# Optimization experiments

Measured on AMD Instinct MI355X. Metric: run time of the kernel, lower is better.

## Reference

```python
import jax, jax.numpy as jnp
import numpy as np

D_MODEL = 1024
NUM_HEADS = 16
D_HEAD = D_MODEL // NUM_HEADS
LN_EPS = 1e-5
ROPE_BASE = 10000.0


def layer_norm(x, w, b=None, eps=LN_EPS):
    mu = jnp.mean(x, axis=-1, keepdims=True)
    var = jnp.mean(jnp.square(x - mu), axis=-1, keepdims=True)
    y = (x - mu) * jax.lax.rsqrt(var + eps) * w
    return y + b if b is not None else y


def _rotate_half(x):
    x1, x2 = jnp.split(x, 2, axis=-1)
    return jnp.concatenate([-x2, x1], axis=-1)


def apply_rotary(q, k):
    # q, k: [B, S, H, Dh]
    s, dh = q.shape[1], q.shape[-1]
    inv_freq = 1.0 / (ROPE_BASE ** (jnp.arange(0, dh, 2, dtype=jnp.float32) / dh))
    t = jnp.arange(s, dtype=jnp.float32)
    freqs = jnp.outer(t, inv_freq)                      # [S, Dh/2]
    emb = jnp.concatenate([freqs, freqs], axis=-1)      # [S, Dh]
    cos = jnp.cos(emb)[None, :, None, :].astype(q.dtype)
    sin = jnp.sin(emb)[None, :, None, :].astype(q.dtype)
    q_rot = q * cos + _rotate_half(q) * sin
    k_rot = k * cos + _rotate_half(k) * sin
    return q_rot, k_rot


def setup_inputs() -> dict:
    key = jax.random.key(0)
    ks = jax.random.split(key, 8)
    B, L, D = 4, 2048, D_MODEL
    x = jax.random.normal(ks[0], (B, L, D), dtype=jnp.float32)
    sequence_id = jnp.sort(jax.random.randint(ks[1], (B, L), 0, 8), axis=-1).astype(jnp.int64)
    scale = 1.0 / np.sqrt(D)
    return {
        "x": x,
        "sequence_id": sequence_id,
        "ln_w": jnp.ones((D,), jnp.float32),
        "ln_b": jnp.zeros((D,), jnp.float32),
        "w_qkv": jax.random.normal(ks[2], (D, 3 * D), jnp.float32) * scale,
        "q_ln_w": jnp.ones((D,), jnp.float32),
        "k_ln_w": jnp.ones((D,), jnp.float32),
        "w_out": jax.random.normal(ks[3], (D, D), jnp.float32) * scale,
    }


def reference(x, sequence_id, ln_w, ln_b, w_qkv, q_ln_w, k_ln_w, w_out):
    B, L, D = x.shape
    H, Dh = NUM_HEADS, D_HEAD
    # fused LayerNorm + QKV projection
    qkv = layer_norm(x, ln_w, ln_b) @ w_qkv              # [B, L, 3D]
    q, k, v = jnp.split(qkv, 3, axis=-1)
    # qk layernorm (scale only, bias=False)
    q = layer_norm(q, q_ln_w)
    k = layer_norm(k, k_ln_w)
    # split heads and apply rotary
    q = q.reshape(B, L, H, Dh)
    k = k.reshape(B, L, H, Dh)
    q, k = apply_rotary(q, k)
    v = v.reshape(B, L, H, Dh)
    # packed-sequence mask: tokens attend only within same sequence id
    mask = (sequence_id[:, :, None] == sequence_id[:, None, :])[:, None, :, :]  # [B,1,L,L]
    scale = 1.0 / np.sqrt(Dh)
    scores = jnp.einsum("bqhd,bkhd->bhqk", q, k) * scale
    scores = jnp.where(mask, scores, jnp.finfo(scores.dtype).min)
    attn = jax.nn.softmax(scores, axis=-1)
    ctx = jnp.einsum("bhqk,bkhd->bqhd", attn, v).reshape(B, L, D)
    return ctx @ w_out
```

## Files before the change

### kernel.cpp

```cpp
#include <hip/hip_runtime.h>
#include <hip/hip_bf16.h>
#include <cstdint>
#include <cstddef>
#include <type_traits>

#define D_MODEL 1024
#define NH      16
#define DH      64
#define LSEQ    2048
#define BATCH   4
#define NTOK    8192
#define K3      3072

typedef __attribute__((ext_vector_type(8))) short  short8;
typedef __attribute__((ext_vector_type(4))) float  floatx4;

__device__ __forceinline__ unsigned short f2bf_bits(float f) {
  __hip_bfloat16 h = __float2bfloat16(f);
  return __builtin_bit_cast(unsigned short, h);
}
__device__ __forceinline__ float bf2f(unsigned short u) {
  return __bfloat162float(__builtin_bit_cast(__hip_bfloat16, u));
}
__device__ __forceinline__ unsigned int pack_bf16(float lo, float hi) {
  return (unsigned int)f2bf_bits(lo) | ((unsigned int)f2bf_bits(hi) << 16);
}

__device__ __forceinline__ void gld_lds16(const void* g, void* l) {
  __builtin_amdgcn_global_load_lds(
      (const __attribute__((address_space(1))) void*)g,
      (__attribute__((address_space(3))) void*)l,
      16, 0, 0);
}

__global__ __launch_bounds__(256)
void transpose_cast(const float* __restrict__ src, __hip_bfloat16* __restrict__ dst,
                    int R, int C) {
  __shared__ float tile[32][33];
  const int c0 = blockIdx.x * 32, r0 = blockIdx.y * 32;
  const int x = threadIdx.x, y = threadIdx.y;
  #pragma unroll
  for (int j = 0; j < 32; j += 8)
    tile[y + j][x] = src[(size_t)(r0 + y + j) * C + c0 + x];
  __syncthreads();
  #pragma unroll
  for (int j = 0; j < 32; j += 8)
    dst[(size_t)(c0 + y + j) * R + r0 + x] = __float2bfloat16(tile[x][y + j]);
}

__global__ __launch_bounds__(256)
void ln_kernel(const float* __restrict__ x, const float* __restrict__ w,
               const float* __restrict__ bb, __hip_bfloat16* __restrict__ h) {
  const int t = blockIdx.x, tid = threadIdx.x;
  const float4 v = reinterpret_cast<const float4*>(x + (size_t)t * D_MODEL)[tid];
  float s  = v.x + v.y + v.z + v.w;
  float ss = v.x*v.x + v.y*v.y + v.z*v.z + v.w*v.w;
  #pragma unroll
  for (int off = 32; off > 0; off >>= 1) {
    s  += __shfl_down(s, off);
    ss += __shfl_down(ss, off);
  }
  __shared__ float red[8];
  if ((tid & 63) == 0) { red[(tid >> 6) * 2] = s; red[(tid >> 6) * 2 + 1] = ss; }
  __syncthreads();
  s  = red[0] + red[2] + red[4] + red[6];
  ss = red[1] + red[3] + red[5] + red[7];
  const float mu  = s * (1.f / D_MODEL);
  const float var = ss * (1.f / D_MODEL) - mu * mu;
  const float rs  = rsqrtf(var + 1e-5f);
  const float4 wv = reinterpret_cast<const float4*>(w)[tid];
  const float4 bv = reinterpret_cast<const float4*>(bb)[tid];
  ushort4 o;
  o.x = f2bf_bits((v.x - mu) * rs * wv.x + bv.x);
  o.y = f2bf_bits((v.y - mu) * rs * wv.y + bv.y);
  o.z = f2bf_bits((v.z - mu) * rs * wv.z + bv.z);
  o.w = f2bf_bits((v.w - mu) * rs * wv.w + bv.w);
  reinterpret_cast<ushort4*>(h + (size_t)t * D_MODEL)[tid] = o;
}

template <typename OutT>
__global__ __launch_bounds__(256, 2)
void gemm_bt(const __hip_bfloat16* __restrict__ A, const __hip_bfloat16* __restrict__ Bt,
             OutT* __restrict__ C, int M, int N, int K) {
  const int tid  = threadIdx.x;
  const int lane = tid & 63;
  const int wave = tid >> 6;
  const int bm = blockIdx.y * 128;
  const int bn = blockIdx.x * 128;
  const int wm = (wave & 1) * 64;
  const int wn = (wave >> 1) * 64;
  const int quad = lane >> 4;
  const int l16  = lane & 15;

  __shared__ __align__(16) __hip_bfloat16 As[128 * 32];
  __shared__ __align__(16) __hip_bfloat16 Bs[128 * 32];

  floatx4 acc[4][4];
  #pragma unroll
  for (int i = 0; i < 4; i++)
    #pragma unroll
    for (int j = 0; j < 4; j++) {
      floatx4 z = {0.f, 0.f, 0.f, 0.f};
      acc[i][j] = z;
    }

  const __hip_bfloat16* Ab = A  + (size_t)bm * K;
  const __hip_bfloat16* Bb = Bt + (size_t)bn * K;
  const int rowa = tid >> 2;
  const int kc   = (tid & 3) * 8;

  for (int k0 = 0; k0 < K; k0 += 32) {
    __syncthreads();
    gld_lds16(Ab + (size_t)rowa        * K + (k0 + kc), (char*)As + tid * 16);
    gld_lds16(Ab + (size_t)(rowa + 64) * K + (k0 + kc), (char*)As + 4096 + tid * 16);
    gld_lds16(Bb + (size_t)rowa        * K + (k0 + kc), (char*)Bs + tid * 16);
    gld_lds16(Bb + (size_t)(rowa + 64) * K + (k0 + kc), (char*)Bs + 4096 + tid * 16);
    __syncthreads();
    short8 af[4], bfr[4];
    #pragma unroll
    for (int i = 0; i < 4; i++)
      af[i] = *reinterpret_cast<const short8*>(As + (wm + i * 16 + l16) * 32 + quad * 8);
    #pragma unroll
    for (int j = 0; j < 4; j++)
      bfr[j] = *reinterpret_cast<const short8*>(Bs + (wn + j * 16 + l16) * 32 + quad * 8);
    #pragma unroll
    for (int i = 0; i < 4; i++)
      #pragma unroll
      for (int j = 0; j < 4; j++)
        acc[i][j] = __builtin_amdgcn_mfma_f32_16x16x32_bf16(af[i], bfr[j], acc[i][j], 0, 0, 0);
  }

  #pragma unroll
  for (int i = 0; i < 4; i++)
    #pragma unroll
    for (int j = 0; j < 4; j++) {
      const int row0 = bm + wm + i * 16 + quad * 4;
      const int col  = bn + wn + j * 16 + l16;
      #pragma unroll
      for (int r = 0; r < 4; r++) {
        if constexpr (std::is_same<OutT, __hip_bfloat16>::value)
          C[(size_t)(row0 + r) * N + col] = __float2bfloat16(acc[i][j][r]);
        else
          C[(size_t)(row0 + r) * N + col] = acc[i][j][r];
      }
    }
}

__global__ __launch_bounds__(256)
void seg_kernel(const int* __restrict__ sid, int* __restrict__ segstart,
                int* __restrict__ segend) {
  const int i = blockIdx.x * 256 + threadIdx.x;
  const int b = i >> 11, l = i & 2047;
  const int* row = sid + (size_t)b * LSEQ;
  const int v = row[l];
  int lo = 0, hi = l;
  while (lo < hi) { int mid = (lo + hi) >> 1; if (row[mid] < v) lo = mid + 1; else hi = mid; }
  segstart[i] = lo;
  lo = l + 1; hi = LSEQ;
  while (lo < hi) { int mid = (lo + hi) >> 1; if (row[mid] <= v) lo = mid + 1; else hi = mid; }
  segend[i] = lo;
}

__global__ __launch_bounds__(256)
void rope_kernel(const unsigned short* __restrict__ qkv, const float* __restrict__ qw,
                 const float* __restrict__ kw, unsigned short* __restrict__ qT,
                 unsigned short* __restrict__ kT, unsigned short* __restrict__ vN) {
  const int t = blockIdx.x, tid = threadIdx.x;
  const int b = t >> 11, l = t & 2047;
  const unsigned short* row = qkv + (size_t)t * K3;
  const ushort4 qu = reinterpret_cast<const ushort4*>(row)[tid];
  const ushort4 ku = reinterpret_cast<const ushort4*>(row + 1024)[tid];
  const ushort4 vu = reinterpret_cast<const ushort4*>(row + 2048)[tid];
  const float4 q4 = make_float4(bf2f(qu.x), bf2f(qu.y), bf2f(qu.z), bf2f(qu.w));
  const float4 k4 = make_float4(bf2f(ku.x), bf2f(ku.y), bf2f(ku.z), bf2f(ku.w));
  float qs  = q4.x + q4.y + q4.z + q4.w;
  float qss = q4.x*q4.x + q4.y*q4.y + q4.z*q4.z + q4.w*q4.w;
  float ks  = k4.x + k4.y + k4.z + k4.w;
  float kss = k4.x*k4.x + k4.y*k4.y + k4.z*k4.z + k4.w*k4.w;
  #pragma unroll
  for (int off = 32; off > 0; off >>= 1) {
    qs  += __shfl_down(qs, off);  qss += __shfl_down(qss, off);
    ks  += __shfl_down(ks, off);  kss += __shfl_down(kss, off);
  }
  __shared__ float red[16];
  const int w = tid >> 6;
  if ((tid & 63) == 0) {
    red[w*4] = qs; red[w*4+1] = qss; red[w*4+2] = ks; red[w*4+3] = kss;
  }
  __syncthreads();
  qs  = red[0] + red[4] + red[8]  + red[12];
  qss = red[1] + red[5] + red[9]  + red[13];
  ks  = red[2] + red[6] + red[10] + red[14];
  kss = red[3] + red[7] + red[11] + red[15];
  const float qmu = qs * (1.f/1024), qvar = qss * (1.f/1024) - qmu*qmu;
  const float qrs = rsqrtf(qvar + 1e-5f);
  const float kmu = ks * (1.f/1024), kvar = kss * (1.f/1024) - kmu*kmu;
  const float krs = rsqrtf(kvar + 1e-5f);

  __shared__ float qn[1024];
  __shared__ float kn[1024];
  const float4 qwv = reinterpret_cast<const float4*>(qw)[tid];
  const float4 kwv = reinterpret_cast<const float4*>(kw)[tid];
  const int d = tid * 4;
  qn[d+0] = (q4.x - qmu) * qrs * qwv.x;
  qn[d+1] = (q4.y - qmu) * qrs * qwv.y;
  qn[d+2] = (q4.z - qmu) * qrs * qwv.z;
  qn[d+3] = (q4.w - qmu) * qrs * qwv.w;
  kn[d+0] = (k4.x - kmu) * krs * kwv.x;
  kn[d+1] = (k4.y - kmu) * krs * kwv.y;
  kn[d+2] = (k4.z - kmu) * krs * kwv.z;
  kn[d+3] = (k4.w - kmu) * krs * kwv.w;
  __syncthreads();

  const int hh = d >> 6, dh = d & 63;
  float oq[4], ok[4];
  #pragma unroll
  for (int i = 0; i < 4; i++) {
    const int dd = dh + i;
    const int j = dd & 31;
    const float th = (float)l * __expf(-(float)j * 0.28782313662425575f);
    const float cs = cosf(th), sn = sinf(th);
    const float qp = (dd < 32) ? -qn[d + i + 32] : qn[d + i - 32];
    const float kp = (dd < 32) ? -kn[d + i + 32] : kn[d + i - 32];
    oq[i] = (qn[d + i] * cs + qp * sn) * 0.125f;
    ok[i] = kn[d + i] * cs + kp * sn;
  }
  const size_t ob = ((size_t)(b * NH + hh) * LSEQ + l) * DH + dh;
  ushort4 pq, pk, pv;
  pq.x = f2bf_bits(oq[0]); pq.y = f2bf_bits(oq[1]); pq.z = f2bf_bits(oq[2]); pq.w = f2bf_bits(oq[3]);
  pk.x = f2bf_bits(ok[0]); pk.y = f2bf_bits(ok[1]); pk.z = f2bf_bits(ok[2]); pk.w = f2bf_bits(ok[3]);
  pv = vu;
  *reinterpret_cast<ushort4*>(qT + ob) = pq;
  *reinterpret_cast<ushort4*>(kT + ob) = pk;
  *reinterpret_cast<ushort4*>(vN + ob) = pv;
}

__global__ __launch_bounds__(256)
void vtrans(const unsigned short* __restrict__ vN, unsigned short* __restrict__ vT) {
  __shared__ __align__(16) unsigned short T[64 * 72];
  const int bh = blockIdx.y;
  const int l0 = blockIdx.x * 64;
  const int tid = threadIdx.x;
  #pragma unroll
  for (int it = 0; it < 2; it++) {
    const int cid = tid + it * 256;
    const int r = cid >> 3, c = (cid & 7) * 8;
    *reinterpret_cast<short8*>(T + r * 72 + c) =
        *reinterpret_cast<const short8*>(vN + ((size_t)bh * LSEQ + l0 + r) * DH + c);
  }
  __syncthreads();
  #pragma unroll
  for (int it = 0; it < 2; it++) {
    const int cid = tid + it * 256;
    const int dh = cid >> 3, c = (cid & 7) * 8;
    short8 o;
    #pragma unroll
    for (int e = 0; e < 8; e++) o[e] = (short)T[(c + e) * 72 + dh];
    *reinterpret_cast<short8*>(vT + ((size_t)bh * DH + dh) * LSEQ + l0 + c) = o;
  }
}

__global__ __launch_bounds__(256)
void attn_mfma(const unsigned short* __restrict__ qT, const unsigned short* __restrict__ kT,
               const unsigned short* __restrict__ vT, const int* __restrict__ segs,
               const int* __restrict__ sege, unsigned short* __restrict__ ctx) {
  const int tid  = threadIdx.x;
  const int lane = tid & 63, w = tid >> 6;
  const int quad = lane >> 4, l16 = lane & 15;
  const int qbase = blockIdx.x * 64;
  const int h = blockIdx.y, b = blockIdx.z;
  const int qy = qbase + w * 16 + l16;
  const size_t bh = (size_t)(b * NH + h);
  const unsigned short* Kg = kT + bh * LSEQ * DH;
  const unsigned short* Vg = vT + bh * DH * LSEQ;

  __shared__ __align__(16) unsigned short Ks[64 * 72];
  __shared__ __align__(16) unsigned short Vs[64 * 72];
  __shared__ __align__(16) unsigned short Ps[4][16 * 72];

  const unsigned short* Qrow = qT + (bh * LSEQ + qy) * DH;
  const short8 qf0 = *reinterpret_cast<const short8*>(Qrow + quad * 8);
  const short8 qf1 = *reinterpret_cast<const short8*>(Qrow + 32 + quad * 8);

  const int st = segs[b * LSEQ + qy];
  const int en = sege[b * LSEQ + qy];
  const unsigned span = (unsigned)(en - st);
  const int kmin = segs[b * LSEQ + qbase] & ~63;
  const int kmax = sege[b * LSEQ + qbase + 63];
  const int wmin = segs[b * LSEQ + qbase + w * 16];
  const int wmax = sege[b * LSEQ + qbase + w * 16 + 15];

  floatx4 acc[4];
  #pragma unroll
  for (int dt = 0; dt < 4; dt++) { floatx4 z = {0.f,0.f,0.f,0.f}; acc[dt] = z; }
  float m = -1e30f, lsum = 0.f;

  const int r_ = tid >> 3, c_ = (tid & 7) * 8;

  for (int kk = kmin; kk < kmax; kk += 64) {
    __syncthreads();
    #pragma unroll
    for (int it = 0; it < 2; it++) {
      const int r = r_ + it * 32;
      *reinterpret_cast<short8*>(Ks + r * 72 + c_) =
          *reinterpret_cast<const short8*>(Kg + (size_t)(kk + r) * DH + c_);
      *reinterpret_cast<short8*>(Vs + r * 72 + c_) =
          *reinterpret_cast<const short8*>(Vg + (size_t)r * LSEQ + kk + c_);
    }
    __syncthreads();

    if (kk + 64 <= wmin || kk >= wmax) continue;

    floatx4 sc[4];
    #pragma unroll
    for (int t = 0; t < 4; t++) {
      const short8 kf0 = *reinterpret_cast<const short8*>(Ks + (t * 16 + l16) * 72 + quad * 8);
      const short8 kf1 = *reinterpret_cast<const short8*>(Ks + (t * 16 + l16) * 72 + 32 + quad * 8);
      floatx4 z = {0.f,0.f,0.f,0.f};
      sc[t] = __builtin_amdgcn_mfma_f32_16x16x32_bf16(kf0, qf0, z, 0, 0, 0);
      sc[t] = __builtin_amdgcn_mfma_f32_16x16x32_bf16(kf1, qf1, sc[t], 0, 0, 0);
    }

    float vm = -1e30f;
    #pragma unroll
    for (int t = 0; t < 4; t++) {
      const int k0 = kk + t * 16 + quad * 4;
      #pragma unroll
      for (int r = 0; r < 4; r++) {
        const bool ok = (unsigned)(k0 + r - st) < span;
        sc[t][r] = ok ? sc[t][r] : -1e30f;
        vm = fmaxf(vm, sc[t][r]);
      }
    }
    vm = fmaxf(vm, __shfl_xor(vm, 16));
    vm = fmaxf(vm, __shfl_xor(vm, 32));
    const float mn = fmaxf(m, vm);
    const float alpha = __expf(m - mn);
    m = mn;

    float rs = 0.f;
    #pragma unroll
    for (int t = 0; t < 4; t++) {
      float p0 = (sc[t][0] > -1e29f) ? __expf(sc[t][0] - mn) : 0.f;
      float p1 = (sc[t][1] > -1e29f) ? __expf(sc[t][1] - mn) : 0.f;
      float p2 = (sc[t][2] > -1e29f) ? __expf(sc[t][2] - mn) : 0.f;
      float p3 = (sc[t][3] > -1e29f) ? __expf(sc[t][3] - mn) : 0.f;
      rs += (p0 + p1) + (p2 + p3);
      uint2 pk;
      pk.x = pack_bf16(p0, p1);
      pk.y = pack_bf16(p2, p3);
      *reinterpret_cast<uint2*>(&Ps[w][l16 * 72 + t * 16 + quad * 4]) = pk;
    }
    rs += __shfl_xor(rs, 16);
    rs += __shfl_xor(rs, 32);
    lsum = lsum * alpha + rs;

    const short8 pf0 = *reinterpret_cast<const short8*>(&Ps[w][l16 * 72 + quad * 8]);
    const short8 pf1 = *reinterpret_cast<const short8*>(&Ps[w][l16 * 72 + 32 + quad * 8]);

    #pragma unroll
    for (int dt = 0; dt < 4; dt++) {
      #pragma unroll
      for (int r = 0; r < 4; r++) acc[dt][r] *= alpha;
      const short8 vf0 = *reinterpret_cast<const short8*>(Vs + (dt * 16 + l16) * 72 + quad * 8);
      const short8 vf1 = *reinterpret_cast<const short8*>(Vs + (dt * 16 + l16) * 72 + 32 + quad * 8);
      acc[dt] = __builtin_amdgcn_mfma_f32_16x16x32_bf16(vf0, pf0, acc[dt], 0, 0, 0);
      acc[dt] = __builtin_amdgcn_mfma_f32_16x16x32_bf16(vf1, pf1, acc[dt], 0, 0, 0);
    }
  }

  const float inv = (lsum > 0.f) ? 1.f / lsum : 0.f;
  unsigned short* orow = ctx + ((size_t)(b * LSEQ + qy)) * D_MODEL + h * DH;
  #pragma unroll
  for (int dt = 0; dt < 4; dt++) {
    uint2 o;
    o.x = pack_bf16(acc[dt][0] * inv, acc[dt][1] * inv);
    o.y = pack_bf16(acc[dt][2] * inv, acc[dt][3] * inv);
    *reinterpret_cast<uint2*>(orow + dt * 16 + quad * 4) = o;
  }
}

extern "C" void kernel_launch(void* const* d_in, const int* in_sizes, int n_in,
                              void* d_out, int out_size, void* d_ws, size_t ws_size,
                              hipStream_t stream) {
  const float* x      = (const float*)d_in[0];
  const int*   sid    = (const int*)d_in[1];
  const float* ln_w   = (const float*)d_in[2];
  const float* ln_b   = (const float*)d_in[3];
  const float* w_qkv  = (const float*)d_in[4];
  const float* q_ln_w = (const float*)d_in[5];
  const float* k_ln_w = (const float*)d_in[6];
  const float* w_out  = (const float*)d_in[7];
  float* out = (float*)d_out;
  char* ws = (char*)d_ws;

  constexpr size_t OFF_WQKVT = 0;
  constexpr size_t OFF_WOUTT = 6291456;
  constexpr size_t OFF_H     = 8388608;
  constexpr size_t OFF_QKV   = 25165824;
  constexpr size_t OFF_QT    = 75497472;
  constexpr size_t OFF_KT    = 92274688;
  constexpr size_t OFF_VN    = 109051904;
  constexpr size_t OFF_VT    = 125829120;
  constexpr size_t OFF_CTX   = 142606336;
  constexpr size_t OFF_SEGS  = 159383552;
  constexpr size_t OFF_SEGE  = 159416320;

  __hip_bfloat16* wqkvT = (__hip_bfloat16*)(ws + OFF_WQKVT);
  __hip_bfloat16* woutT = (__hip_bfloat16*)(ws + OFF_WOUTT);
  __hip_bfloat16* hbuf  = (__hip_bfloat16*)(ws + OFF_H);
  __hip_bfloat16* qkvb  = (__hip_bfloat16*)(ws + OFF_QKV);
  unsigned short* qTb   = (unsigned short*)(ws + OFF_QT);
  unsigned short* kTb   = (unsigned short*)(ws + OFF_KT);
  unsigned short* vNb   = (unsigned short*)(ws + OFF_VN);
  unsigned short* vTb   = (unsigned short*)(ws + OFF_VT);
  unsigned short* ctx   = (unsigned short*)(ws + OFF_CTX);
  int*            segst = (int*)(ws + OFF_SEGS);
  int*            segen = (int*)(ws + OFF_SEGE);

  transpose_cast<<<dim3(96, 32), dim3(32, 8), 0, stream>>>(w_qkv, wqkvT, 1024, 3072);
  transpose_cast<<<dim3(32, 32), dim3(32, 8), 0, stream>>>(w_out, woutT, 1024, 1024);
  ln_kernel<<<NTOK, 256, 0, stream>>>(x, ln_w, ln_b, hbuf);
  gemm_bt<__hip_bfloat16><<<dim3(K3 / 128, NTOK / 128), 256, 0, stream>>>(
      hbuf, wqkvT, qkvb, NTOK, K3, 1024);
  seg_kernel<<<NTOK / 256, 256, 0, stream>>>(sid, segst, segen);
  rope_kernel<<<NTOK, 256, 0, stream>>>((const unsigned short*)qkvb, q_ln_w, k_ln_w,
                                        qTb, kTb, vNb);
  vtrans<<<dim3(LSEQ / 64, BATCH * NH), 256, 0, stream>>>(vNb, vTb);
  attn_mfma<<<dim3(LSEQ / 64, NH, BATCH), 256, 0, stream>>>(qTb, kTb, vTb, segst, segen, ctx);
  gemm_bt<float><<<dim3(D_MODEL / 128, NTOK / 128), 256, 0, stream>>>(
      (const __hip_bfloat16*)ctx, woutT, out, NTOK, D_MODEL, 1024);
}
```

Before: 287.4 us.

## Double GEMM K-tile with XOR-swizzled LDS and read V directly from qkv

The GEMM now stages a 64-wide K slice per iteration instead of 32, which halves the number of barrier pairs. It stores tiles in LDS with an XOR swizzle across 16-byte chunks so the MFMA fragment reads avoid bank conflicts. Separately, the rope kernel no longer copies V into an intermediate head-major buffer; the V transpose kernel reads straight from the packed qkv output, removing a write and a read of a 16 MB buffer. The cost is a larger LDS footprint per block (32 KB), which may limit occupancy under launch_bounds(256,2).

```diff
diff --git a/kernel.cpp b/kernel.cpp
--- a/kernel.cpp
+++ b/kernel.cpp
@@ -92,8 +92,8 @@
   const int quad = lane >> 4;
   const int l16  = lane & 15;
 
-  __shared__ __align__(16) __hip_bfloat16 As[128 * 32];
-  __shared__ __align__(16) __hip_bfloat16 Bs[128 * 32];
+  __shared__ __align__(16) __hip_bfloat16 As[128 * 64];
+  __shared__ __align__(16) __hip_bfloat16 Bs[128 * 64];
 
   floatx4 acc[4][4];
   #pragma unroll
@@ -104,30 +104,38 @@
       acc[i][j] = z;
     }
 
-  const __hip_bfloat16* Ab = A  + (size_t)bm * K;
-  const __hip_bfloat16* Bb = Bt + (size_t)bn * K;
-  const int rowa = tid >> 2;
-  const int kc   = (tid & 3) * 8;
-
-  for (int k0 = 0; k0 < K; k0 += 32) {
+  const int srow = tid >> 3;
+  const int sq   = tid & 7;
+  const int sc8  = (sq ^ (srow & 7)) * 8;
+  const __hip_bfloat16* Ab = A  + (size_t)(bm + srow) * K + sc8;
+  const __hip_bfloat16* Bb = Bt + (size_t)(bn + srow) * K + sc8;
+
+  const int axr = l16 & 7;
+
+  for (int k0 = 0; k0 < K; k0 += 64) {
     __syncthreads();
-    gld_lds16(Ab + (size_t)rowa        * K + (k0 + kc), (char*)As + tid * 16);
-    gld_lds16(Ab + (size_t)(rowa + 64) * K + (k0 + kc), (char*)As + 4096 + tid * 16);
-    gld_lds16(Bb + (size_t)rowa        * K + (k0 + kc), (char*)Bs + tid * 16);
-    gld_lds16(Bb + (size_t)(rowa + 64) * K + (k0 + kc), (char*)Bs + 4096 + tid * 16);
+    #pragma unroll
+    for (int p = 0; p < 4; p++) {
+      gld_lds16(Ab + (size_t)(p * 32) * K + k0, (char*)As + p * 4096 + tid * 16);
+      gld_lds16(Bb + (size_t)(p * 32) * K + k0, (char*)Bs + p * 4096 + tid * 16);
+    }
     __syncthreads();
-    short8 af[4], bfr[4];
-    #pragma unroll
-    for (int i = 0; i < 4; i++)
-      af[i] = *reinterpret_cast<const short8*>(As + (wm + i * 16 + l16) * 32 + quad * 8);
-    #pragma unroll
-    for (int j = 0; j < 4; j++)
-      bfr[j] = *reinterpret_cast<const short8*>(Bs + (wn + j * 16 + l16) * 32 + quad * 8);
-    #pragma unroll
-    for (int i = 0; i < 4; i++)
+    #pragma unroll
+    for (int s0 = 0; s0 < 2; s0++) {
+      const int qo = ((s0 * 4 + quad) ^ axr) * 8;
+      short8 af[4], bfr[4];
+      #pragma unroll
+      for (int i = 0; i < 4; i++)
+        af[i] = *reinterpret_cast<const short8*>(As + (wm + i * 16 + l16) * 64 + qo);
       #pragma unroll
       for (int j = 0; j < 4; j++)
-        acc[i][j] = __builtin_amdgcn_mfma_f32_16x16x32_bf16(af[i], bfr[j], acc[i][j], 0, 0, 0);
+        bfr[j] = *reinterpret_cast<const short8*>(Bs + (wn + j * 16 + l16) * 64 + qo);
+      #pragma unroll
+      for (int i = 0; i < 4; i++)
+        #pragma unroll
+        for (int j = 0; j < 4; j++)
+          acc[i][j] = __builtin_amdgcn_mfma_f32_16x16x32_bf16(af[i], bfr[j], acc[i][j], 0, 0, 0);
+    }
   }
 
   #pragma unroll
@@ -164,13 +172,12 @@
 __global__ __launch_bounds__(256)
 void rope_kernel(const unsigned short* __restrict__ qkv, const float* __restrict__ qw,
                  const float* __restrict__ kw, unsigned short* __restrict__ qT,
-                 unsigned short* __restrict__ kT, unsigned short* __restrict__ vN) {
+                 unsigned short* __restrict__ kT) {
   const int t = blockIdx.x, tid = threadIdx.x;
   const int b = t >> 11, l = t & 2047;
   const unsigned short* row = qkv + (size_t)t * K3;
   const ushort4 qu = reinterpret_cast<const ushort4*>(row)[tid];
   const ushort4 ku = reinterpret_cast<const ushort4*>(row + 1024)[tid];
-  const ushort4 vu = reinterpret_cast<const ushort4*>(row + 2048)[tid];
   const float4 q4 = make_float4(bf2f(qu.x), bf2f(qu.y), bf2f(qu.z), bf2f(qu.w));
   const float4 k4 = make_float4(bf2f(ku.x), bf2f(ku.y), bf2f(ku.z), bf2f(ku.w));
   float qs  = q4.x + q4.y + q4.z + q4.w;
@@ -226,19 +233,18 @@
     ok[i] = kn[d + i] * cs + kp * sn;
   }
   const size_t ob = ((size_t)(b * NH + hh) * LSEQ + l) * DH + dh;
-  ushort4 pq, pk, pv;
+  ushort4 pq, pk;
   pq.x = f2bf_bits(oq[0]); pq.y = f2bf_bits(oq[1]); pq.z = f2bf_bits(oq[2]); pq.w = f2bf_bits(oq[3]);
   pk.x = f2bf_bits(ok[0]); pk.y = f2bf_bits(ok[1]); pk.z = f2bf_bits(ok[2]); pk.w = f2bf_bits(ok[3]);
-  pv = vu;
   *reinterpret_cast<ushort4*>(qT + ob) = pq;
   *reinterpret_cast<ushort4*>(kT + ob) = pk;
-  *reinterpret_cast<ushort4*>(vN + ob) = pv;
-}
-
-__global__ __launch_bounds__(256)
-void vtrans(const unsigned short* __restrict__ vN, unsigned short* __restrict__ vT) {
+}
+
+__global__ __launch_bounds__(256)
+void vtrans(const unsigned short* __restrict__ qkv, unsigned short* __restrict__ vT) {
   __shared__ __align__(16) unsigned short T[64 * 72];
   const int bh = blockIdx.y;
+  const int b = bh >> 4, h = bh & 15;
   const int l0 = blockIdx.x * 64;
   const int tid = threadIdx.x;
   #pragma unroll
@@ -246,7 +252,8 @@
     const int cid = tid + it * 256;
     const int r = cid >> 3, c = (cid & 7) * 8;
     *reinterpret_cast<short8*>(T + r * 72 + c) =
-        *reinterpret_cast<const short8*>(vN + ((size_t)bh * LSEQ + l0 + r) * DH + c);
+        *reinterpret_cast<const short8*>(qkv + (size_t)(b * LSEQ + l0 + r) * K3
+                                         + 2048 + h * DH + c);
   }
   __syncthreads();
   #pragma unroll
@@ -400,11 +407,10 @@
   constexpr size_t OFF_QKV   = 25165824;
   constexpr size_t OFF_QT    = 75497472;
   constexpr size_t OFF_KT    = 92274688;
-  constexpr size_t OFF_VN    = 109051904;
-  constexpr size_t OFF_VT    = 125829120;
-  constexpr size_t OFF_CTX   = 142606336;
-  constexpr size_t OFF_SEGS  = 159383552;
-  constexpr size_t OFF_SEGE  = 159416320;
+  constexpr size_t OFF_VT    = 109051904;
+  constexpr size_t OFF_CTX   = 125829120;
+  constexpr size_t OFF_SEGS  = 142606336;
+  constexpr size_t OFF_SEGE  = 142639104;
 
   __hip_bfloat16* wqkvT = (__hip_bfloat16*)(ws + OFF_WQKVT);
   __hip_bfloat16* woutT = (__hip_bfloat16*)(ws + OFF_WOUTT);
@@ -412,7 +418,6 @@
   __hip_bfloat16* qkvb  = (__hip_bfloat16*)(ws + OFF_QKV);
   unsigned short* qTb   = (unsigned short*)(ws + OFF_QT);
   unsigned short* kTb   = (unsigned short*)(ws + OFF_KT);
-  unsigned short* vNb   = (unsigned short*)(ws + OFF_VN);
   unsigned short* vTb   = (unsigned short*)(ws + OFF_VT);
   unsigned short* ctx   = (unsigned short*)(ws + OFF_CTX);
   int*            segst = (int*)(ws + OFF_SEGS);
@@ -425,8 +430,8 @@
       hbuf, wqkvT, qkvb, NTOK, K3, 1024);
   seg_kernel<<<NTOK / 256, 256, 0, stream>>>(sid, segst, segen);
   rope_kernel<<<NTOK, 256, 0, stream>>>((const unsigned short*)qkvb, q_ln_w, k_ln_w,
-                                        qTb, kTb, vNb);
-  vtrans<<<dim3(LSEQ / 64, BATCH * NH), 256, 0, stream>>>(vNb, vTb);
+                                        qTb, kTb);
+  vtrans<<<dim3(LSEQ / 64, BATCH * NH), 256, 0, stream>>>((const unsigned short*)qkvb, vTb);
   attn_mfma<<<dim3(LSEQ / 64, NH, BATCH), 256, 0, stream>>>(qTb, kTb, vTb, segst, segen, ctx);
   gemm_bt<float><<<dim3(D_MODEL / 128, NTOK / 128), 256, 0, stream>>>(
       (const __hip_bfloat16*)ctx, woutT, out, NTOK, D_MODEL, 1024);
```

After: 279.3 us. 1.03x faster.
